# Kernel tuning notes

Measured on AMD Instinct MI355X. Metric: run time of the kernel, lower is better.

Reference implementation:

```python
import jax, jax.numpy as jnp
import numpy as np

THRESH = 0.4


def setup_inputs() -> dict:
    key = jax.random.key(0)
    ks = jax.random.split(key, 8)
    B, N, C, H, O = 8, 16384, 640, 256, 128
    s = 0.02  # small init so sigmoid(logits) ~ 0.5 -> realistic mixed selection
    return {
        "point_features": jax.random.normal(ks[0], (B, N, C), jnp.float32),
        "point_coords": jax.random.normal(ks[1], (B, N, 3), jnp.float32) * 10.0,
        "w1": jax.random.normal(ks[2], (C, H), jnp.float32) * s,
        "b1": jnp.zeros((H,), jnp.float32),
        "w2": jax.random.normal(ks[3], (H, 1), jnp.float32) * s,
        "b2": jnp.zeros((1,), jnp.float32),
        "wo": jax.random.normal(ks[4], (C, O), jnp.float32) * s,
        "bo": jnp.zeros((O,), jnp.float32),
    }


def reference(point_features, point_coords, w1, b1, w2, b2, wo, bo):
    B, N, _ = point_features.shape
    # 2-layer MLP -> per-point logit -> sigmoid score
    h = jax.nn.relu(jnp.einsum('bnc,ch->bnh', point_features, w1) + b1)
    logits = jnp.einsum('bnh,ho->bno', h, w2) + b2          # [B, N, 1]
    scores = jax.nn.sigmoid(logits)                          # [B, N, 1]
    # score-scaled features through output projection
    feats = jnp.einsum('bnc,co->bno', point_features * scores, wo) + bo  # [B, N, O]
    # score-threshold selection + per-batch stream compaction into a
    # zero-padded tensor (padded to N, the jit-static worst case)
    sel = scores[..., 0] > THRESH                            # [B, N] bool
    pos = jnp.cumsum(sel.astype(jnp.int32), axis=1) - 1      # destination slot
    pos = jnp.where(sel, pos, N)                             # unselected -> OOB (dropped)
    bidx = jnp.arange(B)[:, None]
    selected_keypoints = jnp.zeros_like(feats).at[bidx, pos].set(feats, mode='drop')
    selected_coords = jnp.zeros_like(point_coords).at[bidx, pos].set(point_coords, mode='drop')
    # point_mask: True where the row is zero padding (matches (coords==0).sum(-1)!=0)
    point_mask = jnp.sum(selected_coords == 0, axis=-1) != 0
    return selected_keypoints, selected_coords, point_mask
```

## Files before the change

### kernel.cpp

```cpp
#include <hip/hip_runtime.h>
#include <hip/hip_bf16.h>


typedef __attribute__((ext_vector_type(8))) short short8v;
typedef __attribute__((ext_vector_type(4))) float f32x4;

#define M_TOTAL 131072
#define C_DIM 640
#define H_DIM 256
#define O_DIM 128
#define NCOMB 384
#define TM 64
#define KSTEPS 20
#define N_PTS 16384
#define TILES_PER_B 256
#define NTILES 2048
#define THRL -0.4054651081f
#define FIX_MARGIN 0.03f

#define OUT_COORD_OFF 16777216
#define OUT_MASK_OFF  17170432

#define WT_OFF     0u
#define TMASK_OFF  491520u
#define TAGG_OFF   507904u
#define TEXCL_OFF  516096u
#define COUNTS_OFF 524288u
#define G_OFF      1572864u

#define VMCNT(n) asm volatile("s_waitcnt vmcnt(" #n ")" ::: "memory")
#define LGKMCNT0 asm volatile("s_waitcnt lgkmcnt(0)" ::: "memory")

__device__ __forceinline__ int swzB(int u) { return u ^ ((u >> 3) & 7); }

__device__ __forceinline__ void glds16(const void* g, void* l) {
  const __attribute__((address_space(1))) unsigned int* gp =
      reinterpret_cast<const __attribute__((address_space(1))) unsigned int*>(
          reinterpret_cast<uintptr_t>(g));
  __attribute__((address_space(3))) unsigned int* lp =
      reinterpret_cast<__attribute__((address_space(3))) unsigned int*>(
          reinterpret_cast<uintptr_t>(l));
  __builtin_amdgcn_global_load_lds(gp, lp, 16, 0, 0);
}

__device__ __forceinline__ unsigned int f2bf_bits(float f) {
  unsigned int u = __builtin_bit_cast(unsigned int, f);
  return (u + 0x7fffu + ((u >> 16) & 1u)) >> 16;
}
__device__ __forceinline__ unsigned int pack_bf2(float lo, float hi) {
  return f2bf_bits(lo) | (f2bf_bits(hi) << 16);
}

__global__ __launch_bounds__(256) void convert_w(const float* __restrict__ w1,
                                                 const float* __restrict__ wo,
                                                 unsigned short* __restrict__ Wt2) {
  int o = blockIdx.x * 256 + threadIdx.x;
  if (o < NCOMB * C_DIM) {
    int e = o & 7;
    int chunk = o >> 3;
    int ks = chunk / 1536;
    int r = chunk - ks * 1536;
    int u = swzB(r);
    int n = u >> 2, kg = u & 3;
    int k = ks * 32 + kg * 8 + e;
    float v = (n < H_DIM) ? w1[k * H_DIM + n] : wo[k * O_DIM + (n - H_DIM)];
    Wt2[o] = (unsigned short)f2bf_bits(v);
  }
}

__global__ __launch_bounds__(512, 4) void gemm_fused(
    const float* __restrict__ pf, const unsigned short* __restrict__ Wt2,
    const float* __restrict__ w1, const float* __restrict__ b1,
    const float* __restrict__ w2, const float* __restrict__ b2,
    const float* __restrict__ bo, unsigned long long* __restrict__ tmask,
    int* __restrict__ tagg, float* __restrict__ G) {
  __shared__ __align__(16) unsigned short As[2][2048];
  __shared__ __align__(16) unsigned short Bs[3][12288];

  const int tid = threadIdx.x;
  const int lane = tid & 63;
  const int wv = tid >> 6;
  const int q = lane & 15;
  const int p = lane >> 4;
  const int tile = blockIdx.x;
  const int m0 = tile * TM;

  f32x4 acc[3][4];
#pragma unroll
  for (int i = 0; i < 3; ++i)
#pragma unroll
    for (int rt = 0; rt < 4; ++rt) acc[i][rt] = (f32x4){0.f, 0.f, 0.f, 0.f};

  const float* asrc = pf + (size_t)(m0 + (tid >> 3)) * C_DIM + (tid & 7) * 4;
  const int aphys = ((tid >> 1) ^ ((tid >> 4) & 3)) * 8 + (tid & 1) * 4;
  const int aswz = (q >> 1) & 3;

  float4 Rcur, Rnext;
  {
    Rcur = *(const float4*)(asrc);
#pragma unroll
    for (int u = 0; u < 3; ++u)
      glds16(Wt2 + (size_t)(u * 512 + tid) * 8, &Bs[0][(u * 512 + tid) * 8]);
    Rnext = *(const float4*)(asrc + 32);
#pragma unroll
    for (int u = 0; u < 3; ++u)
      glds16(Wt2 + (size_t)(1536 + u * 512 + tid) * 8, &Bs[1][(u * 512 + tid) * 8]);
    *(uint2*)&As[0][aphys] = make_uint2(pack_bf2(Rcur.x, Rcur.y), pack_bf2(Rcur.z, Rcur.w));
    Rcur = Rnext;
  }

#pragma unroll
  for (int t = 0; t < KSTEPS; ++t) {
    if (t < KSTEPS - 1) { VMCNT(4); } else { VMCNT(0); }
    LGKMCNT0;
    __builtin_amdgcn_s_barrier();
    __builtin_amdgcn_sched_barrier(0);
    if (t + 2 < KSTEPS) {
      Rnext = *(const float4*)(asrc + (t + 2) * 32);
#pragma unroll
      for (int u = 0; u < 3; ++u)
        glds16(Wt2 + (size_t)((t + 2) * 1536 + u * 512 + tid) * 8,
               &Bs[(t + 2) % 3][(u * 512 + tid) * 8]);
      __builtin_amdgcn_sched_barrier(0);
    }
    if (t + 1 < KSTEPS) {
      *(uint2*)&As[(t + 1) & 1][aphys] =
          make_uint2(pack_bf2(Rcur.x, Rcur.y), pack_bf2(Rcur.z, Rcur.w));
      Rcur = Rnext;
    }
    short8v af[4];
#pragma unroll
    for (int rt = 0; rt < 4; ++rt)
      af[rt] = *(const short8v*)&As[t & 1][((rt * 64 + q * 4 + p) ^ aswz) * 8];
    __builtin_amdgcn_s_setprio(1);
#pragma unroll
    for (int i = 0; i < 3; ++i) {
      const int ub = (((wv + 8 * i) * 16 + q) << 2) + p;
      short8v bfv = *(const short8v*)&Bs[t % 3][swzB(ub) * 8];
#pragma unroll
      for (int rt = 0; rt < 4; ++rt)
        acc[i][rt] = __builtin_amdgcn_mfma_f32_16x16x32_bf16(af[rt], bfv, acc[i][rt], 0, 0, 0);
    }
    __builtin_amdgcn_s_setprio(0);
  }
  __syncthreads();

  float* lpart = (float*)&As[0][0];
  float* llog = (float*)&Bs[0][0];
  float* srow = llog + 64;
  float* fsum = srow + 64;
  unsigned long long* s_fixmask = (unsigned long long*)(fsum + 4);

  float w2v[2], b1v[2];
#pragma unroll
  for (int i = 0; i < 2; ++i) {
    int col = (wv + 8 * i) * 16 + q;
    w2v[i] = w2[col];
    b1v[i] = b1[col];
  }
#pragma unroll
  for (int rt = 0; rt < 4; ++rt) {
    float pr[4] = {0.f, 0.f, 0.f, 0.f};
#pragma unroll
    for (int i = 0; i < 2; ++i)
#pragma unroll
      for (int r = 0; r < 4; ++r)
        pr[r] += fmaxf(acc[i][rt][r] + b1v[i], 0.f) * w2v[i];
#pragma unroll
    for (int mk = 1; mk < 16; mk <<= 1)
#pragma unroll
      for (int r = 0; r < 4; ++r) pr[r] += __shfl_xor(pr[r], mk);
    if (q == 0)
#pragma unroll
      for (int r = 0; r < 4; ++r) lpart[wv * 64 + rt * 16 + p * 4 + r] = pr[r];
  }
  __syncthreads();

  bool nf = false;
  if (wv == 0) {
    float lg = b2[0];
#pragma unroll
    for (int w = 0; w < 8; ++w) lg += lpart[w * 64 + tid];
    llog[tid] = lg;
    nf = fabsf(lg - THRL) < FIX_MARGIN;
  }
  unsigned long long fm = __ballot(nf);
  if (tid == 0) *s_fixmask = fm;
  __syncthreads();

  unsigned long long fixmask = *s_fixmask;
  while (fixmask) {
    int row = __ffsll(fixmask) - 1;
    fixmask &= fixmask - 1;
    if (tid < 256) {
      const float* prow = pf + (size_t)(m0 + row) * C_DIM;
      float a0 = 0.f, a1 = 0.f;
      for (int c = 0; c < C_DIM; c += 2) {
        a0 = fmaf(prow[c], w1[(size_t)c * H_DIM + tid], a0);
        a1 = fmaf(prow[c + 1], w1[(size_t)(c + 1) * H_DIM + tid], a1);
      }
      float v = fmaxf(a0 + a1 + b1[tid], 0.f) * w2[tid];
#pragma unroll
      for (int mk = 1; mk < 64; mk <<= 1) v += __shfl_xor(v, mk);
      if (lane == 0) fsum[wv] = v;
    }
    __syncthreads();
    if (tid == 0)
      llog[row] = fsum[0] + fsum[1] + fsum[2] + fsum[3] + b2[0];
    __syncthreads();
  }

  bool sel = false;
  float flog = 0.f;
  if (wv == 0) {
    flog = llog[tid];
    sel = flog > THRL;
  }
  unsigned long long selmask = __ballot(sel);
  if (wv == 0) {
    srow[tid] = 1.f / (1.f + expf(-flog));
    if (tid == 0) {
      tmask[tile] = selmask;
      tagg[tile] = __popcll(selmask);
    }
  }
  __syncthreads();

  {
    const int gcol = wv * 16 + q;
    const float bov = bo[gcol];
#pragma unroll
    for (int rt = 0; rt < 4; ++rt)
#pragma unroll
      for (int r = 0; r < 4; ++r) {
        int row = rt * 16 + p * 4 + r;
        G[(size_t)(m0 + row) * O_DIM + gcol] = fmaf(acc[2][rt][r], srow[row], bov);
      }
  }
}

__global__ __launch_bounds__(256) void scan_tiles(const int* __restrict__ tagg,
                                                  int* __restrict__ texcl,
                                                  int* __restrict__ counts) {
  __shared__ int wsum[4];
  const int c = blockIdx.x, t = threadIdx.x;
  const int lane = t & 63, w = t >> 6;
  int v = tagg[c * 256 + t];
  int inc = v;
#pragma unroll
  for (int d = 1; d < 64; d <<= 1) {
    int n = __shfl_up(inc, d);
    if (lane >= d) inc += n;
  }
  if (lane == 63) wsum[w] = inc;
  __syncthreads();
  int base = 0;
#pragma unroll
  for (int ww = 0; ww < 4; ++ww)
    if (ww < w) base += wsum[ww];
  texcl[c * 256 + t] = base + inc - v;
  if (t == 255) counts[c] = base + inc;
}

__global__ __launch_bounds__(512) void scatter(
    const float* __restrict__ G, const unsigned long long* __restrict__ tmask,
    const int* __restrict__ texcl, const float* __restrict__ pc,
    float* __restrict__ out) {
  const int tile = blockIdx.x;
  const int tid = threadIdx.x;
  const int lane = tid & 63;
  const int wv = tid >> 6;
  const unsigned long long mask = tmask[tile];
  const int base = (tile >> 8) * N_PTS + texcl[tile];
  const int m0 = tile * TM;
#pragma unroll
  for (int j = 0; j < 8; ++j) {
    const int row = wv * 8 + j;
    if (!((mask >> row) & 1ull)) continue;
    const int dst = base + __popcll(mask & ((1ull << row) - 1ull));
    const int m = m0 + row;
    float2 g = *(const float2*)(G + (size_t)m * O_DIM + lane * 2);
    *(float2*)(out + (size_t)dst * O_DIM + lane * 2) = g;
    if (lane == 0) {
      float c0 = pc[m * 3], c1 = pc[m * 3 + 1], c2 = pc[m * 3 + 2];
      float* oc = out + OUT_COORD_OFF;
      oc[dst * 3] = c0; oc[dst * 3 + 1] = c1; oc[dst * 3 + 2] = c2;
      out[OUT_MASK_OFF + dst] = (c0 == 0.f || c1 == 0.f || c2 == 0.f) ? 1.f : 0.f;
    }
  }
}

__global__ __launch_bounds__(256) void fill_tail(const int* __restrict__ counts,
                                                 float* __restrict__ out) {
  int m = blockIdx.x * 4 + (threadIdx.x >> 6);
  int lane = threadIdx.x & 63;
  int b = m >> 14, j = m & (N_PTS - 1);
  if (j < counts[b]) return;
  *(float2*)(out + (size_t)m * O_DIM + lane * 2) = make_float2(0.f, 0.f);
  if (lane == 0) {
    float* oc = out + OUT_COORD_OFF;
    oc[m * 3] = 0.f; oc[m * 3 + 1] = 0.f; oc[m * 3 + 2] = 0.f;
    out[OUT_MASK_OFF + m] = 1.f;
  }
}

extern "C" void kernel_launch(void* const* d_in, const int* in_sizes, int n_in,
                              void* d_out, int out_size, void* d_ws, size_t ws_size,
                              hipStream_t stream) {
  const float* pf = (const float*)d_in[0];
  const float* pc = (const float*)d_in[1];
  const float* w1 = (const float*)d_in[2];
  const float* b1 = (const float*)d_in[3];
  const float* w2 = (const float*)d_in[4];
  const float* b2 = (const float*)d_in[5];
  const float* wo = (const float*)d_in[6];
  const float* bo = (const float*)d_in[7];
  float* out = (float*)d_out;
  char* ws = (char*)d_ws;

  unsigned short* Wt2 = (unsigned short*)(ws + WT_OFF);
  unsigned long long* tmask = (unsigned long long*)(ws + TMASK_OFF);
  int* tagg = (int*)(ws + TAGG_OFF);
  int* texcl = (int*)(ws + TEXCL_OFF);
  int* counts = (int*)(ws + COUNTS_OFF);
  float* G = (float*)(ws + G_OFF);

  convert_w<<<960, 256, 0, stream>>>(w1, wo, Wt2);
  gemm_fused<<<NTILES, 512, 0, stream>>>(pf, Wt2, w1, b1, w2, b2, bo,
                                         tmask, tagg, G);
  scan_tiles<<<8, 256, 0, stream>>>(tagg, texcl, counts);
  scatter<<<NTILES, 512, 0, stream>>>(G, tmask, texcl, pc, out);
  fill_tail<<<M_TOTAL / 4, 256, 0, stream>>>(counts, out);
}
```

Measured before the change: 197.4 us.

## Split GEMM K-step into two MFMA phases with interleaved LDS loads; grid-stride fill_tail

Each K-step of the fused GEMM main loop now runs as two halves. The first half issues MFMAs for row tiles 0-1 while the next global loads are in flight. The second half loads the remaining A fragments, writes the next A tile to LDS, and then runs the MFMAs for row tiles 2-3, with extra barriers around each phase so LDS reads overlap matrix math better. Separately, fill_tail launches 2048 blocks that stride over rows instead of one block per four rows, which cuts launch and block-scheduling overhead. The extra barriers per K-step could cost more than the overlap they buy.

Result: no change. 193.7 us (-1.9%).

```diff
diff --git a/kernel.cpp b/kernel.cpp
--- a/kernel.cpp
+++ b/kernel.cpp
@@ -30,6 +30,8 @@
 
 #define VMCNT(n) asm volatile("s_waitcnt vmcnt(" #n ")" ::: "memory")
 #define LGKMCNT0 asm volatile("s_waitcnt lgkmcnt(0)" ::: "memory")
+#define SBAR __builtin_amdgcn_s_barrier()
+#define SCHED0 __builtin_amdgcn_sched_barrier(0)
 
 __device__ __forceinline__ int swzB(int u) { return u ^ ((u >> 3) & 7); }
 
@@ -97,51 +99,71 @@
 
   float4 Rcur, Rnext;
   {
-    Rcur = *(const float4*)(asrc);
+    float4 R0 = *(const float4*)(asrc);
 #pragma unroll
     for (int u = 0; u < 3; ++u)
       glds16(Wt2 + (size_t)(u * 512 + tid) * 8, &Bs[0][(u * 512 + tid) * 8]);
-    Rnext = *(const float4*)(asrc + 32);
 #pragma unroll
     for (int u = 0; u < 3; ++u)
       glds16(Wt2 + (size_t)(1536 + u * 512 + tid) * 8, &Bs[1][(u * 512 + tid) * 8]);
-    *(uint2*)&As[0][aphys] = make_uint2(pack_bf2(Rcur.x, Rcur.y), pack_bf2(Rcur.z, Rcur.w));
-    Rcur = Rnext;
+    Rcur = *(const float4*)(asrc + 32);
+    *(uint2*)&As[0][aphys] = make_uint2(pack_bf2(R0.x, R0.y), pack_bf2(R0.z, R0.w));
+    LGKMCNT0;
+    VMCNT(4);
+    SBAR;
   }
 
 #pragma unroll
   for (int t = 0; t < KSTEPS; ++t) {
-    if (t < KSTEPS - 1) { VMCNT(4); } else { VMCNT(0); }
-    LGKMCNT0;
-    __builtin_amdgcn_s_barrier();
-    __builtin_amdgcn_sched_barrier(0);
+    short8v af01[2], af23[2], bf[3];
+#pragma unroll
+    for (int rt = 0; rt < 2; ++rt)
+      af01[rt] = *(const short8v*)&As[t & 1][((rt * 64 + q * 4 + p) ^ aswz) * 8];
+#pragma unroll
+    for (int i = 0; i < 3; ++i) {
+      const int ub = (((wv + 8 * i) * 16 + q) << 2) + p;
+      bf[i] = *(const short8v*)&Bs[t % 3][swzB(ub) * 8];
+    }
     if (t + 2 < KSTEPS) {
       Rnext = *(const float4*)(asrc + (t + 2) * 32);
 #pragma unroll
       for (int u = 0; u < 3; ++u)
         glds16(Wt2 + (size_t)((t + 2) * 1536 + u * 512 + tid) * 8,
                &Bs[(t + 2) % 3][(u * 512 + tid) * 8]);
-      __builtin_amdgcn_sched_barrier(0);
-    }
+    }
+    SBAR;
+    LGKMCNT0;
+    SCHED0;
+    __builtin_amdgcn_s_setprio(1);
+#pragma unroll
+    for (int i = 0; i < 3; ++i)
+#pragma unroll
+      for (int rt = 0; rt < 2; ++rt)
+        acc[i][rt] = __builtin_amdgcn_mfma_f32_16x16x32_bf16(af01[rt], bf[i],
+                                                             acc[i][rt], 0, 0, 0);
+    __builtin_amdgcn_s_setprio(0);
+    SBAR;
+#pragma unroll
+    for (int rt = 2; rt < 4; ++rt)
+      af23[rt - 2] = *(const short8v*)&As[t & 1][((rt * 64 + q * 4 + p) ^ aswz) * 8];
     if (t + 1 < KSTEPS) {
       *(uint2*)&As[(t + 1) & 1][aphys] =
           make_uint2(pack_bf2(Rcur.x, Rcur.y), pack_bf2(Rcur.z, Rcur.w));
       Rcur = Rnext;
     }
-    short8v af[4];
-#pragma unroll
-    for (int rt = 0; rt < 4; ++rt)
-      af[rt] = *(const short8v*)&As[t & 1][((rt * 64 + q * 4 + p) ^ aswz) * 8];
+    LGKMCNT0;
+    if (t + 2 < KSTEPS) { VMCNT(4); } else { VMCNT(0); }
+    SBAR;
+    SCHED0;
     __builtin_amdgcn_s_setprio(1);
 #pragma unroll
-    for (int i = 0; i < 3; ++i) {
-      const int ub = (((wv + 8 * i) * 16 + q) << 2) + p;
-      short8v bfv = *(const short8v*)&Bs[t % 3][swzB(ub) * 8];
-#pragma unroll
-      for (int rt = 0; rt < 4; ++rt)
-        acc[i][rt] = __builtin_amdgcn_mfma_f32_16x16x32_bf16(af[rt], bfv, acc[i][rt], 0, 0, 0);
-    }
+    for (int i = 0; i < 3; ++i)
+#pragma unroll
+      for (int rt = 2; rt < 4; ++rt)
+        acc[i][rt] = __builtin_amdgcn_mfma_f32_16x16x32_bf16(af23[rt - 2], bf[i],
+                                                             acc[i][rt], 0, 0, 0);
     __builtin_amdgcn_s_setprio(0);
+    SBAR;
   }
   __syncthreads();
 
@@ -292,15 +314,16 @@
 
 __global__ __launch_bounds__(256) void fill_tail(const int* __restrict__ counts,
                                                  float* __restrict__ out) {
-  int m = blockIdx.x * 4 + (threadIdx.x >> 6);
-  int lane = threadIdx.x & 63;
-  int b = m >> 14, j = m & (N_PTS - 1);
-  if (j < counts[b]) return;
-  *(float2*)(out + (size_t)m * O_DIM + lane * 2) = make_float2(0.f, 0.f);
-  if (lane == 0) {
-    float* oc = out + OUT_COORD_OFF;
-    oc[m * 3] = 0.f; oc[m * 3 + 1] = 0.f; oc[m * 3 + 2] = 0.f;
-    out[OUT_MASK_OFF + m] = 1.f;
+  const int lane = threadIdx.x & 63;
+  for (int m = blockIdx.x * 4 + (threadIdx.x >> 6); m < M_TOTAL; m += 8192) {
+    int b = m >> 14, j = m & (N_PTS - 1);
+    if (j < counts[b]) continue;
+    *(float2*)(out + (size_t)m * O_DIM + lane * 2) = make_float2(0.f, 0.f);
+    if (lane == 0) {
+      float* oc = out + OUT_COORD_OFF;
+      oc[m * 3] = 0.f; oc[m * 3 + 1] = 0.f; oc[m * 3 + 2] = 0.f;
+      out[OUT_MASK_OFF + m] = 1.f;
+    }
   }
 }
 
@@ -330,5 +353,5 @@
                                          tmask, tagg, G);
   scan_tiles<<<8, 256, 0, stream>>>(tagg, texcl, counts);
   scatter<<<NTILES, 512, 0, stream>>>(G, tmask, texcl, pc, out);
-  fill_tail<<<M_TOTAL / 4, 256, 0, stream>>>(counts, out);
-}
+  fill_tail<<<2048, 256, 0, stream>>>(counts, out);
+}
```
